# Optimization experiments

Measured on AMD Instinct MI355X. Metric: run time of the kernel, lower is better.

The kernel has to match this reference:

```python
import jax, jax.numpy as jnp
import numpy as np

C_M = 256
C = 32
C_Z = 128
EPS = 1e-5


def setup_inputs() -> dict:
    key = jax.random.key(0)
    ks = jax.random.split(key, 8)
    b, s, i = 1, 128, 256
    msa = jax.random.normal(ks[0], (b, s, i, C_M), dtype=jnp.float32)
    scale_in = 1.0 / np.sqrt(C_M)
    scale_out = 1.0 / np.sqrt(C * C)
    return {
        "msa_representation": msa,
        "ln_w": jnp.ones((C_M,), jnp.float32),
        "ln_b": jnp.zeros((C_M,), jnp.float32),
        "w_left": jax.random.normal(ks[1], (C_M, C), jnp.float32) * scale_in,
        "b_left": jax.random.normal(ks[2], (C,), jnp.float32) * scale_in,
        "w_right": jax.random.normal(ks[3], (C_M, C), jnp.float32) * scale_in,
        "b_right": jax.random.normal(ks[4], (C,), jnp.float32) * scale_in,
        "w_out": jax.random.normal(ks[5], (C * C, C_Z), jnp.float32) * scale_out,
        "b_out": jax.random.normal(ks[6], (C_Z,), jnp.float32) * scale_out,
    }


def reference(msa_representation, ln_w, ln_b, w_left, b_left, w_right, b_right, w_out, b_out):
    x = msa_representation
    # LayerNorm over c_m
    mu = jnp.mean(x, axis=-1, keepdims=True)
    var = jnp.mean(jnp.square(x - mu), axis=-1, keepdims=True)
    x = (x - mu) * jax.lax.rsqrt(var + EPS) * ln_w + ln_b
    # dual projections: [b, s, i, c]
    A = x @ w_left + b_left
    B = x @ w_right + b_right
    s_dim = x.shape[1]
    # outer product mean over MSA depth s: [b, i, j, c, c]
    outer = jnp.einsum('bsic,bsjd->bijcd', A, B) / s_dim
    b_, i_, j_ = outer.shape[0], outer.shape[1], outer.shape[2]
    flat = outer.reshape(b_, i_, j_, C * C)
    return flat @ w_out + b_out
```

## Files before the change

kernel.cpp:

```cpp
#include <hip/hip_runtime.h>

typedef __attribute__((ext_vector_type(8))) short short8;
typedef __attribute__((ext_vector_type(4))) float f32x4;

#define CM 256
#define CC 32
#define CZ 128
#define SDIM 128
#define IDIM 256

__device__ __forceinline__ unsigned short f2bf(float f) {
  union { float f; unsigned u; } v; v.f = f;
  unsigned r = v.u + 0x7fffu + ((v.u >> 16) & 1u);
  return (unsigned short)(r >> 16);
}

__global__ void k_prep(const float* __restrict__ wl, const float* __restrict__ wr,
                       const float* __restrict__ wo,
                       unsigned short* __restrict__ wlrT, unsigned short* __restrict__ WF) {
  int t = blockIdx.x * 256 + threadIdx.x;
  if (t < 64 * 256) {
    int c = t >> 8, e = t & 255;
    float v = (c < CC) ? wl[e * CC + c] : wr[e * CC + (c - CC)];
    wlrT[c * 256 + e] = f2bf(v);
  } else {
    int t2 = t - 64 * 256;
    if (t2 < 8 * 32 * 64) {
      int zt = t2 >> 11, ks = (t2 >> 6) & 31, lane = t2 & 63;
      int ln = lane & 15, qd = lane >> 4;
      int z = zt * 16 + ln;
#pragma unroll
      for (int e = 0; e < 8; ++e) {
        int c = qd * 8 + e, d = ks;
        WF[(size_t)t2 * 8 + e] = f2bf(wo[(c * 32 + d) * CZ + z] * (1.0f / 128.0f));
      }
    }
  }
}

__global__ __launch_bounds__(512) void k_lnproj(
    const float* __restrict__ x, const float* __restrict__ lnw, const float* __restrict__ lnb,
    const float* __restrict__ bl, const float* __restrict__ br,
    const unsigned short* __restrict__ wlrT,
    unsigned short* __restrict__ Abuf, unsigned short* __restrict__ Bbuf) {
  extern __shared__ __align__(16) char lds[];
  unsigned short* xn = (unsigned short*)lds;
  unsigned short* sT = (unsigned short*)(lds + 67584);
  int tid = threadIdx.x;
  int lane = tid & 63, ww = tid >> 6;
  int qd = lane >> 4, ln = lane & 15;
  int i = blockIdx.x;

  for (int rr = 0; rr < 16; ++rr) {
    int s = ww * 16 + rr;
    float4 v = ((const float4*)(x + ((size_t)s * IDIM + i) * CM))[lane];
    float s1 = v.x + v.y + v.z + v.w;
    float s2 = v.x * v.x + v.y * v.y + v.z * v.z + v.w * v.w;
#pragma unroll
    for (int off = 32; off; off >>= 1) {
      s1 += __shfl_xor(s1, off);
      s2 += __shfl_xor(s2, off);
    }
    float mu = s1 * (1.0f / 256.0f);
    float var = s2 * (1.0f / 256.0f) - mu * mu;
    float rs = rsqrtf(var + 1e-5f);
    float4 w4 = ((const float4*)lnw)[lane];
    float4 b4 = ((const float4*)lnb)[lane];
    ushort4 h;
    h.x = f2bf((v.x - mu) * rs * w4.x + b4.x);
    h.y = f2bf((v.y - mu) * rs * w4.y + b4.y);
    h.z = f2bf((v.z - mu) * rs * w4.z + b4.z);
    h.w = f2bf((v.w - mu) * rs * w4.w + b4.w);
    *(ushort4*)&xn[s * 264 + lane * 4] = h;
  }
  __syncthreads();

  f32x4 acc[4];
#pragma unroll
  for (int nt = 0; nt < 4; ++nt) acc[nt] = (f32x4){0.f, 0.f, 0.f, 0.f};
#pragma unroll
  for (int ks = 0; ks < 8; ++ks) {
    short8 af = *(const short8*)&xn[(ww * 16 + ln) * 264 + ks * 32 + qd * 8];
#pragma unroll
    for (int nt = 0; nt < 4; ++nt) {
      short8 bf = *(const short8*)(wlrT + (nt * 16 + ln) * 256 + ks * 32 + qd * 8);
      acc[nt] = __builtin_amdgcn_mfma_f32_16x16x32_bf16(af, bf, acc[nt], 0, 0, 0);
    }
  }
#pragma unroll
  for (int nt = 0; nt < 4; ++nt) {
    int c64 = nt * 16 + ln;
    float bias = (c64 < CC) ? bl[c64] : br[c64 - CC];
    ushort4 h;
    h.x = f2bf(acc[nt][0] + bias);
    h.y = f2bf(acc[nt][1] + bias);
    h.z = f2bf(acc[nt][2] + bias);
    h.w = f2bf(acc[nt][3] + bias);
    *(ushort4*)&sT[c64 * 136 + ww * 16 + qd * 4] = h;
  }
  __syncthreads();

#pragma unroll
  for (int k = 0; k < 2; ++k) {
    int idx = tid + k * 512;
    int row = idx >> 4, ch = idx & 15;
    short8 v = *(const short8*)&sT[row * 136 + ch * 8];
    unsigned short* dst = (row < CC) ? (Abuf + ((size_t)(i * CC + row)) * SDIM)
                                     : (Bbuf + ((size_t)(i * CC + row - CC)) * SDIM);
    *(short8*)(dst + ch * 8) = v;
  }
}

__global__ __launch_bounds__(1024) void k_main(
    const unsigned short* __restrict__ Abuf, const unsigned short* __restrict__ Bbuf,
    const unsigned short* __restrict__ WF, const float* __restrict__ bout,
    float* __restrict__ out) {
  extern __shared__ __align__(16) char lds[];
  unsigned short* sA = (unsigned short*)lds;
  unsigned short* sB = sA + 256 * 136;
  unsigned short* sP = (unsigned short*)lds;
  float* redF = (float*)lds;
  int tid = threadIdx.x;
  int lane = tid & 63, ww = tid >> 6;
  int qd = lane >> 4, ln = lane & 15;
  int i0 = blockIdx.x * 8, j0 = blockIdx.y * 8;

  {
    int row = tid >> 4, ch = tid & 15;
#pragma unroll
    for (int it = 0; it < 4; ++it) {
      int r = it * 64 + row;
      short8 va = *(const short8*)(Abuf + (size_t)(i0 * CC + r) * SDIM + ch * 8);
      short8 vb = *(const short8*)(Bbuf + (size_t)(j0 * CC + r) * SDIM + ch * 8);
      *(short8*)&sA[r * 136 + ch * 8] = va;
      *(short8*)&sB[r * 136 + ch * 8] = vb;
    }
  }
  __syncthreads();

  int wy = ww >> 2, wx = ww & 3;
  f32x4 acc1[4][4];
  for (int a = 0; a < 4; ++a)
    for (int b = 0; b < 4; ++b) acc1[a][b] = (f32x4){0.f, 0.f, 0.f, 0.f};
#pragma unroll
  for (int ks = 0; ks < 4; ++ks) {
    short8 af[4];
#pragma unroll
    for (int ti = 0; ti < 4; ++ti)
      af[ti] = *(const short8*)&sA[(wy * 64 + ti * 16 + ln) * 136 + ks * 32 + qd * 8];
#pragma unroll
    for (int tj = 0; tj < 4; ++tj) {
      short8 bf = *(const short8*)&sB[(wx * 64 + tj * 16 + ln) * 136 + ks * 32 + qd * 8];
#pragma unroll
      for (int ti = 0; ti < 4; ++ti)
        acc1[ti][tj] = __builtin_amdgcn_mfma_f32_16x16x32_bf16(af[ti], bf, acc1[ti][tj], 0, 0, 0);
    }
  }
  __syncthreads();

#pragma unroll
  for (int ti = 0; ti < 4; ++ti) {
    int m0 = wy * 64 + ti * 16;
    int iloc = m0 >> 5;
    int cbase = (m0 & 31) + qd * 4;
    int cb8 = cbase >> 3;
#pragma unroll
    for (int tj = 0; tj < 4; ++tj) {
      int n0 = wx * 64 + tj * 16;
      int jloc = n0 >> 5;
      int d = (n0 & 31) + ln;
      int p = iloc * 8 + jloc;
      ushort4 h;
      h.x = f2bf(acc1[ti][tj][0]);
      h.y = f2bf(acc1[ti][tj][1]);
      h.z = f2bf(acc1[ti][tj][2]);
      h.w = f2bf(acc1[ti][tj][3]);
      *(ushort4*)&sP[p * 1032 + d * 32 + ((cb8 ^ (d & 3)) * 8) + (cbase & 7)] = h;
    }
  }
  __syncthreads();

  int zt2 = ww & 3, ksq = ww >> 2;
  f32x4 acc2[4][2];
#pragma unroll
  for (int mt = 0; mt < 4; ++mt)
#pragma unroll
    for (int h2 = 0; h2 < 2; ++h2) acc2[mt][h2] = (f32x4){0.f, 0.f, 0.f, 0.f};
#pragma unroll
  for (int kk = 0; kk < 8; ++kk) {
    int ks = ksq * 8 + kk;
    short8 bfr[2];
#pragma unroll
    for (int h2 = 0; h2 < 2; ++h2)
      bfr[h2] = *(const short8*)(WF + ((size_t)((zt2 * 2 + h2) * 32 + ks) * 64 + lane) * 8);
    short8 afr[4];
#pragma unroll
    for (int mt = 0; mt < 4; ++mt)
      afr[mt] = *(const short8*)&sP[(mt * 16 + ln) * 1032 + ks * 32 + ((qd ^ (ks & 3)) * 8)];
#pragma unroll
    for (int mt = 0; mt < 4; ++mt)
#pragma unroll
      for (int h2 = 0; h2 < 2; ++h2)
        acc2[mt][h2] = __builtin_amdgcn_mfma_f32_16x16x32_bf16(afr[mt], bfr[h2], acc2[mt][h2], 0, 0, 0);
  }

  __syncthreads();
  if (ksq >= 2) {
#pragma unroll
    for (int mt = 0; mt < 4; ++mt)
#pragma unroll
      for (int h2 = 0; h2 < 2; ++h2)
#pragma unroll
        for (int rg = 0; rg < 4; ++rg) {
          int p = mt * 16 + qd * 4 + rg, zl = h2 * 16 + ln;
          redF[((zt2 * 2 + (ksq - 2)) * 64 + p) * 33 + zl] = acc2[mt][h2][rg];
        }
  }
  __syncthreads();
  if (ksq < 2) {
#pragma unroll
    for (int mt = 0; mt < 4; ++mt)
#pragma unroll
      for (int h2 = 0; h2 < 2; ++h2)
#pragma unroll
        for (int rg = 0; rg < 4; ++rg) {
          int p = mt * 16 + qd * 4 + rg, zl = h2 * 16 + ln;
          acc2[mt][h2][rg] += redF[((zt2 * 2 + ksq) * 64 + p) * 33 + zl];
        }
    if (ksq == 1) {
#pragma unroll
      for (int mt = 0; mt < 4; ++mt)
#pragma unroll
        for (int h2 = 0; h2 < 2; ++h2)
#pragma unroll
          for (int rg = 0; rg < 4; ++rg) {
            int p = mt * 16 + qd * 4 + rg, zl = h2 * 16 + ln;
            redF[((zt2 * 2 + 1) * 64 + p) * 33 + zl] = acc2[mt][h2][rg];
          }
    }
  }
  __syncthreads();
  if (ksq == 0) {
#pragma unroll
    for (int mt = 0; mt < 4; ++mt)
#pragma unroll
      for (int h2 = 0; h2 < 2; ++h2) {
        int z = (zt2 * 2 + h2) * 16 + ln;
        float bz = bout[z];
#pragma unroll
        for (int rg = 0; rg < 4; ++rg) {
          int p = mt * 16 + qd * 4 + rg, zl = h2 * 16 + ln;
          float v = acc2[mt][h2][rg] + redF[((zt2 * 2 + 1) * 64 + p) * 33 + zl] + bz;
          int i = i0 + (p >> 3), j = j0 + (p & 7);
          out[((size_t)i * IDIM + j) * CZ + z] = v;
        }
      }
  }
}

extern "C" void kernel_launch(void* const* d_in, const int* in_sizes, int n_in,
                              void* d_out, int out_size, void* d_ws, size_t ws_size,
                              hipStream_t stream) {
  const float* msa = (const float*)d_in[0];
  const float* lnw = (const float*)d_in[1];
  const float* lnb = (const float*)d_in[2];
  const float* wl  = (const float*)d_in[3];
  const float* bl  = (const float*)d_in[4];
  const float* wr  = (const float*)d_in[5];
  const float* br  = (const float*)d_in[6];
  const float* wo  = (const float*)d_in[7];
  const float* bo  = (const float*)d_in[8];
  float* out = (float*)d_out;

  char* ws = (char*)d_ws;
  unsigned short* Abuf = (unsigned short*)ws;
  unsigned short* Bbuf = (unsigned short*)(ws + (2u << 20));
  unsigned short* wlrT = (unsigned short*)(ws + (4u << 20));
  unsigned short* WF   = (unsigned short*)(ws + (4u << 20) + 32768);

  (void)hipFuncSetAttribute((const void*)k_main,
                            hipFuncAttributeMaxDynamicSharedMemorySize, 139264);
  (void)hipFuncSetAttribute((const void*)k_lnproj,
                            hipFuncAttributeMaxDynamicSharedMemorySize, 84992);

  k_prep<<<128, 256, 0, stream>>>(wl, wr, wo, wlrT, WF);
  k_lnproj<<<256, 512, 84992, stream>>>(msa, lnw, lnb, bl, br, wlrT, Abuf, Bbuf);
  k_main<<<dim3(32, 32), 1024, 139264, stream>>>(Abuf, Bbuf, WF, bo, out);
}
```

Before: 155.9 us.

## Shrink main kernel tile and LDS, load A fragments from global

The main kernel now works on 8x4 (i,j) tiles with 512 threads and about 34 KB of LDS instead of 8x8 tiles with 1024 threads and 136 KB, so several blocks can share a CU. The left projection is stored pre-swizzled in MFMA fragment order, so A operands are read straight from global memory without staging in LDS. The second GEMM runs in two halves over the c dimension, with only four waves doing it and a two-way reduction at the end. The intent is higher occupancy and less LDS traffic, at the cost of more grid blocks, repeated global reads of A and the weight fragments, and half the waves sitting idle during the output GEMM.

```diff
diff --git a/kernel.cpp b/kernel.cpp
--- a/kernel.cpp
+++ b/kernel.cpp
@@ -42,7 +42,7 @@
     const float* __restrict__ x, const float* __restrict__ lnw, const float* __restrict__ lnb,
     const float* __restrict__ bl, const float* __restrict__ br,
     const unsigned short* __restrict__ wlrT,
-    unsigned short* __restrict__ Abuf, unsigned short* __restrict__ Bbuf) {
+    unsigned short* __restrict__ A2, unsigned short* __restrict__ Bbuf) {
   extern __shared__ __align__(16) char lds[];
   unsigned short* xn = (unsigned short*)lds;
   unsigned short* sT = (unsigned short*)(lds + 67584);
@@ -100,54 +100,52 @@
   }
   __syncthreads();
 
-#pragma unroll
-  for (int k = 0; k < 2; ++k) {
-    int idx = tid + k * 512;
-    int row = idx >> 4, ch = idx & 15;
-    short8 v = *(const short8*)&sT[row * 136 + ch * 8];
-    unsigned short* dst = (row < CC) ? (Abuf + ((size_t)(i * CC + row)) * SDIM)
-                                     : (Bbuf + ((size_t)(i * CC + row - CC)) * SDIM);
-    *(short8*)(dst + ch * 8) = v;
-  }
-}
-
-__global__ __launch_bounds__(1024) void k_main(
-    const unsigned short* __restrict__ Abuf, const unsigned short* __restrict__ Bbuf,
+  {
+    int rtloc = ww >> 2, ks4 = ww & 3;
+    short8 v = *(const short8*)&sT[(rtloc * 16 + ln) * 136 + ks4 * 32 + qd * 8];
+    *(short8*)(A2 + ((size_t)(((2 * i + rtloc) * 4 + ks4) * 64 + lane)) * 8) = v;
+  }
+  {
+    int row = tid >> 4, ch = tid & 15;
+    short8 v = *(const short8*)&sT[(CC + row) * 136 + ch * 8];
+    *(short8*)(Bbuf + ((size_t)(i * CC + row)) * SDIM + ch * 8) = v;
+  }
+}
+
+__global__ __launch_bounds__(512, 4) void k_main(
+    const unsigned short* __restrict__ A2, const unsigned short* __restrict__ Bbuf,
     const unsigned short* __restrict__ WF, const float* __restrict__ bout,
     float* __restrict__ out) {
   extern __shared__ __align__(16) char lds[];
-  unsigned short* sA = (unsigned short*)lds;
-  unsigned short* sB = sA + 256 * 136;
+  unsigned short* sB = (unsigned short*)lds;
   unsigned short* sP = (unsigned short*)lds;
   float* redF = (float*)lds;
   int tid = threadIdx.x;
   int lane = tid & 63, ww = tid >> 6;
   int qd = lane >> 4, ln = lane & 15;
-  int i0 = blockIdx.x * 8, j0 = blockIdx.y * 8;
-
-  {
-    int row = tid >> 4, ch = tid & 15;
-#pragma unroll
-    for (int it = 0; it < 4; ++it) {
-      int r = it * 64 + row;
-      short8 va = *(const short8*)(Abuf + (size_t)(i0 * CC + r) * SDIM + ch * 8);
-      short8 vb = *(const short8*)(Bbuf + (size_t)(j0 * CC + r) * SDIM + ch * 8);
-      *(short8*)&sA[r * 136 + ch * 8] = va;
-      *(short8*)&sB[r * 136 + ch * 8] = vb;
-    }
-  }
-  __syncthreads();
-
-  int wy = ww >> 2, wx = ww & 3;
+  int i0 = blockIdx.x * 8, j0 = blockIdx.y * 4;
+
+#pragma unroll
+  for (int t = 0; t < 4; ++t) {
+    int idx = tid + t * 512;
+    int r = idx >> 4, ch = idx & 15;
+    short8 v = *(const short8*)(Bbuf + (size_t)(j0 * CC + r) * SDIM + ch * 8);
+    *(short8*)&sB[r * 136 + ch * 8] = v;
+  }
+  __syncthreads();
+
+  int wy = ww >> 1, wx = ww & 1;
   f32x4 acc1[4][4];
+#pragma unroll
   for (int a = 0; a < 4; ++a)
+#pragma unroll
     for (int b = 0; b < 4; ++b) acc1[a][b] = (f32x4){0.f, 0.f, 0.f, 0.f};
 #pragma unroll
   for (int ks = 0; ks < 4; ++ks) {
     short8 af[4];
 #pragma unroll
     for (int ti = 0; ti < 4; ++ti)
-      af[ti] = *(const short8*)&sA[(wy * 64 + ti * 16 + ln) * 136 + ks * 32 + qd * 8];
+      af[ti] = *(const short8*)(A2 + ((size_t)((i0 * 2 + wy * 4 + ti) * 4 + ks) * 64 + lane) * 8);
 #pragma unroll
     for (int tj = 0; tj < 4; ++tj) {
       short8 bf = *(const short8*)&sB[(wx * 64 + tj * 16 + ln) * 136 + ks * 32 + qd * 8];
@@ -156,103 +154,83 @@
         acc1[ti][tj] = __builtin_amdgcn_mfma_f32_16x16x32_bf16(af[ti], bf, acc1[ti][tj], 0, 0, 0);
     }
   }
-  __syncthreads();
-
-#pragma unroll
-  for (int ti = 0; ti < 4; ++ti) {
-    int m0 = wy * 64 + ti * 16;
-    int iloc = m0 >> 5;
-    int cbase = (m0 & 31) + qd * 4;
-    int cb8 = cbase >> 3;
-#pragma unroll
-    for (int tj = 0; tj < 4; ++tj) {
-      int n0 = wx * 64 + tj * 16;
-      int jloc = n0 >> 5;
-      int d = (n0 & 31) + ln;
-      int p = iloc * 8 + jloc;
-      ushort4 h;
-      h.x = f2bf(acc1[ti][tj][0]);
-      h.y = f2bf(acc1[ti][tj][1]);
-      h.z = f2bf(acc1[ti][tj][2]);
-      h.w = f2bf(acc1[ti][tj][3]);
-      *(ushort4*)&sP[p * 1032 + d * 32 + ((cb8 ^ (d & 3)) * 8) + (cbase & 7)] = h;
-    }
-  }
-  __syncthreads();
-
-  int zt2 = ww & 3, ksq = ww >> 2;
-  f32x4 acc2[4][2];
-#pragma unroll
-  for (int mt = 0; mt < 4; ++mt)
-#pragma unroll
-    for (int h2 = 0; h2 < 2; ++h2) acc2[mt][h2] = (f32x4){0.f, 0.f, 0.f, 0.f};
-#pragma unroll
-  for (int kk = 0; kk < 8; ++kk) {
-    int ks = ksq * 8 + kk;
-    short8 bfr[2];
-#pragma unroll
-    for (int h2 = 0; h2 < 2; ++h2)
-      bfr[h2] = *(const short8*)(WF + ((size_t)((zt2 * 2 + h2) * 32 + ks) * 64 + lane) * 8);
-    short8 afr[4];
-#pragma unroll
-    for (int mt = 0; mt < 4; ++mt)
-      afr[mt] = *(const short8*)&sP[(mt * 16 + ln) * 1032 + ks * 32 + ((qd ^ (ks & 3)) * 8)];
-#pragma unroll
-    for (int mt = 0; mt < 4; ++mt)
-#pragma unroll
-      for (int h2 = 0; h2 < 2; ++h2)
-        acc2[mt][h2] = __builtin_amdgcn_mfma_f32_16x16x32_bf16(afr[mt], bfr[h2], acc2[mt][h2], 0, 0, 0);
-  }
-
-  __syncthreads();
-  if (ksq >= 2) {
-#pragma unroll
-    for (int mt = 0; mt < 4; ++mt)
-#pragma unroll
-      for (int h2 = 0; h2 < 2; ++h2)
+
+  f32x4 acc2[2][4];
+#pragma unroll
+  for (int mt = 0; mt < 2; ++mt)
+#pragma unroll
+    for (int z4 = 0; z4 < 4; ++z4) acc2[mt][z4] = (f32x4){0.f, 0.f, 0.f, 0.f};
+
+  for (int h = 0; h < 2; ++h) {
+    __syncthreads();
+#pragma unroll
+    for (int ti = 0; ti < 4; ++ti) {
+      int iloc = 2 * wy + (ti >> 1);
+      int cbase = 16 * (ti & 1) + qd * 4;
+      int cb = cbase >> 3;
+#pragma unroll
+      for (int u = 0; u < 2; ++u) {
+        int tj = h + u * 2;
+        int jloc = 2 * wx + (tj >> 1);
+        int p = iloc * 4 + jloc;
+        ushort4 hh;
+        hh.x = f2bf(acc1[ti][tj][0]);
+        hh.y = f2bf(acc1[ti][tj][1]);
+        hh.z = f2bf(acc1[ti][tj][2]);
+        hh.w = f2bf(acc1[ti][tj][3]);
+        *(ushort4*)&sP[p * 520 + ln * 32 + ((((ln >> 1) & 3) ^ cb) * 8) + (cbase & 7)] = hh;
+      }
+    }
+    __syncthreads();
+    if (ww < 4) {
+      int zth = ww & 1, kq = ww >> 1;
+#pragma unroll
+      for (int kk = 0; kk < 8; ++kk) {
+        int ksp = kq * 8 + kk;
+        int gks = h * 16 + ksp;
+        short8 afr[2];
+#pragma unroll
+        for (int mt = 0; mt < 2; ++mt)
+          afr[mt] = *(const short8*)&sP[(mt * 16 + ln) * 520 + ksp * 32 + ((((ksp >> 1) & 3) ^ qd) * 8)];
+#pragma unroll
+        for (int z4 = 0; z4 < 4; ++z4) {
+          int zt = zth * 4 + z4;
+          short8 bfr = *(const short8*)(WF + ((size_t)(zt * 32 + gks) * 64 + lane) * 8);
+#pragma unroll
+          for (int mt = 0; mt < 2; ++mt)
+            acc2[mt][z4] = __builtin_amdgcn_mfma_f32_16x16x32_bf16(afr[mt], bfr, acc2[mt][z4], 0, 0, 0);
+        }
+      }
+    }
+  }
+
+  __syncthreads();
+  if (ww == 2 || ww == 3) {
+    int zth = ww & 1;
+#pragma unroll
+    for (int mt = 0; mt < 2; ++mt)
+#pragma unroll
+      for (int z4 = 0; z4 < 4; ++z4)
 #pragma unroll
         for (int rg = 0; rg < 4; ++rg) {
-          int p = mt * 16 + qd * 4 + rg, zl = h2 * 16 + ln;
-          redF[((zt2 * 2 + (ksq - 2)) * 64 + p) * 33 + zl] = acc2[mt][h2][rg];
+          int p = mt * 16 + qd * 4 + rg;
+          redF[(zth * 32 + p) * 68 + z4 * 16 + ln] = acc2[mt][z4][rg];
         }
   }
   __syncthreads();
-  if (ksq < 2) {
-#pragma unroll
-    for (int mt = 0; mt < 4; ++mt)
-#pragma unroll
-      for (int h2 = 0; h2 < 2; ++h2)
+  if (ww == 0 || ww == 1) {
+    int zth = ww & 1;
+#pragma unroll
+    for (int mt = 0; mt < 2; ++mt)
+#pragma unroll
+      for (int z4 = 0; z4 < 4; ++z4) {
+        int z = (zth * 4 + z4) * 16 + ln;
+        float bz = bout[z];
 #pragma unroll
         for (int rg = 0; rg < 4; ++rg) {
-          int p = mt * 16 + qd * 4 + rg, zl = h2 * 16 + ln;
-          acc2[mt][h2][rg] += redF[((zt2 * 2 + ksq) * 64 + p) * 33 + zl];
-        }
-    if (ksq == 1) {
-#pragma unroll
-      for (int mt = 0; mt < 4; ++mt)
-#pragma unroll
-        for (int h2 = 0; h2 < 2; ++h2)
-#pragma unroll
-          for (int rg = 0; rg < 4; ++rg) {
-            int p = mt * 16 + qd * 4 + rg, zl = h2 * 16 + ln;
-            redF[((zt2 * 2 + 1) * 64 + p) * 33 + zl] = acc2[mt][h2][rg];
-          }
-    }
-  }
-  __syncthreads();
-  if (ksq == 0) {
-#pragma unroll
-    for (int mt = 0; mt < 4; ++mt)
-#pragma unroll
-      for (int h2 = 0; h2 < 2; ++h2) {
-        int z = (zt2 * 2 + h2) * 16 + ln;
-        float bz = bout[z];
-#pragma unroll
-        for (int rg = 0; rg < 4; ++rg) {
-          int p = mt * 16 + qd * 4 + rg, zl = h2 * 16 + ln;
-          float v = acc2[mt][h2][rg] + redF[((zt2 * 2 + 1) * 64 + p) * 33 + zl] + bz;
-          int i = i0 + (p >> 3), j = j0 + (p & 7);
-          out[((size_t)i * IDIM + j) * CZ + z] = v;
+          int p = mt * 16 + qd * 4 + rg;
+          float v = acc2[mt][z4][rg] + redF[(zth * 32 + p) * 68 + z4 * 16 + ln] + bz;
+          out[((size_t)(i0 + (p >> 2)) * IDIM + (j0 + (p & 3))) * CZ + z] = v;
         }
       }
   }
@@ -273,17 +251,15 @@
   float* out = (float*)d_out;
 
   char* ws = (char*)d_ws;
-  unsigned short* Abuf = (unsigned short*)ws;
+  unsigned short* A2   = (unsigned short*)ws;
   unsigned short* Bbuf = (unsigned short*)(ws + (2u << 20));
   unsigned short* wlrT = (unsigned short*)(ws + (4u << 20));
   unsigned short* WF   = (unsigned short*)(ws + (4u << 20) + 32768);
 
-  (void)hipFuncSetAttribute((const void*)k_main,
-                            hipFuncAttributeMaxDynamicSharedMemorySize, 139264);
   (void)hipFuncSetAttribute((const void*)k_lnproj,
                             hipFuncAttributeMaxDynamicSharedMemorySize, 84992);
 
   k_prep<<<128, 256, 0, stream>>>(wl, wr, wo, wlrT, WF);
-  k_lnproj<<<256, 512, 84992, stream>>>(msa, lnw, lnb, bl, br, wlrT, Abuf, Bbuf);
-  k_main<<<dim3(32, 32), 1024, 139264, stream>>>(Abuf, Bbuf, WF, bo, out);
-}
+  k_lnproj<<<256, 512, 84992, stream>>>(msa, lnw, lnb, bl, br, wlrT, A2, Bbuf);
+  k_main<<<dim3(32, 64), 512, 34816, stream>>>(A2, Bbuf, WF, bo, out);
+}
```

Result: faster. 152.2 us (-2.4%).
